# Performance work log

Measured on AMD Instinct MI355X. Metric: run time of the kernel, lower is better.

## Reference

```python
import jax, jax.numpy as jnp
import numpy as np

NEG = -9e15  # sentinel used by the torch module for masked logits


def setup_inputs() -> dict:
    key = jax.random.key(0)
    k_x, k_nl, k_q, k_k, k_v = jax.random.split(key, 5)
    n, m, nhid = 50000, 16, 128
    x = jax.random.normal(k_x, (n, nhid), dtype=jnp.float32)
    neighbor_list = jax.random.randint(k_nl, (n, m), 0, n)  # value n-1 == padding
    # xavier_uniform with gain=1.414 for square (nhid, nhid) matrices
    bound = 1.414 * np.sqrt(6.0 / (nhid + nhid))
    Q = jax.random.uniform(k_q, (nhid, nhid), jnp.float32, -bound, bound)
    K = jax.random.uniform(k_k, (nhid, nhid), jnp.float32, -bound, bound)
    V = jax.random.uniform(k_v, (nhid, nhid), jnp.float32, -bound, bound)
    return {"x": x, "neighbor_list": neighbor_list, "Q": Q, "K": K, "V": V}


def _forward(x, neighbor_list, Q, K, V):
    n, nhid = x.shape
    scare = jnp.asarray(nhid ** 0.5, x.dtype)
    # masks: neighbor index n-1 means padding
    mask = (neighbor_list != n - 1).astype(x.dtype)            # (n, m)
    mask1 = mask[:, :, None] * mask[:, None, :]                # (n, m, m)
    mask2 = jnp.concatenate([jnp.ones((n, 1), x.dtype), mask], axis=1)[:, None, :]  # (n,1,m+1)

    # ---- stage 1: neighbor-level attention ----
    nm = x[neighbor_list]                                      # (n, m, h) gather
    Qn = jnp.einsum('nmk,kh->nmh', nm, Q)
    Kn = jnp.einsum('nmk,kh->nmh', nm, K)
    Vn = jnp.einsum('nmk,kh->nmh', nm, V)
    s = jnp.einsum('nih,njh->nij', Qn, Kn)                     # (n, m, m)
    s = jax.nn.leaky_relu(s, 0.01)
    s = jnp.where(mask1 > 0, s, NEG) * scare                   # faithful: scale after mask
    a = jax.nn.softmax(s, axis=2)                              # dropout is identity (eval)
    nres = jnp.einsum('nij,njh->nih', a, Vn)                   # (n, m, h)

    # ---- stage 2: node-level attention over [self, neighbors] ----
    xr = x[:, None, :]                                         # (n, 1, h)
    cat = jnp.concatenate([xr, nres], axis=1)                  # (n, m+1, h)
    Qx = jnp.einsum('nik,kh->nih', xr, Q)                      # (n, 1, h)
    Kc = jnp.einsum('njk,kh->njh', cat, K)
    Vc = jnp.einsum('njk,kh->njh', cat, V)
    s2 = jnp.einsum('nih,njh->nij', Qx, Kc) * scare            # (n, 1, m+1)
    s2 = jax.nn.leaky_relu(s2, 0.01)
    s2 = jnp.where(mask2 > 0, s2, NEG)
    a2 = jax.nn.softmax(s2, axis=2)
    out = jnp.einsum('nij,njh->nih', a2, Vc)[:, 0, :]          # (n, h)

    # F.normalize: L2 along dim 1, eps 1e-12
    norm = jnp.linalg.norm(out, axis=1, keepdims=True)
    return out / jnp.maximum(norm, 1e-12)


def reference(x, neighbor_list, Q, K, V):
    return _forward(x, neighbor_list, Q, K, V)
```

## Files before the change

### kernel.cpp

```cpp
#include <hip/hip_runtime.h>
#include <math.h>

#define NEG_CONST (-9000000000000000.0f)
#define SCARE 11.313708498984761f

#define DPP_XOR1  0xB1
#define DPP_XOR2  0x4E
#define DPP_XOR7  0x141
#define DPP_XOR15 0x140

template<int CTRL>
__device__ __forceinline__ float dpp_add(float x) {
    int yi = __builtin_amdgcn_update_dpp(0, __float_as_int(x), CTRL, 0xF, 0xF, true);
    return x + __int_as_float(yi);
}
template<int CTRL>
__device__ __forceinline__ float dpp_max(float x) {
    int yi = __builtin_amdgcn_update_dpp(0, __float_as_int(x), CTRL, 0xF, 0xF, true);
    return fmaxf(x, __int_as_float(yi));
}

__device__ __forceinline__ void wave_lds_fence() {
    __builtin_amdgcn_wave_barrier();
    asm volatile("s_waitcnt lgkmcnt(0)" ::: "memory");
    __builtin_amdgcn_wave_barrier();
}
__device__ __forceinline__ void wave_vm_fence() {
    __builtin_amdgcn_wave_barrier();
    asm volatile("s_waitcnt vmcnt(0) lgkmcnt(0)" ::: "memory");
    __builtin_amdgcn_wave_barrier();
}

__global__ __launch_bounds__(256) void small_mm_qkt(const float* __restrict__ Q,
                                                    const float* __restrict__ K,
                                                    float* __restrict__ QKt) {
    int r  = blockIdx.x * 8 + (threadIdx.x >> 5);
    int c0 = (threadIdx.x & 31) * 4;
    float a0 = 0.f, a1 = 0.f, a2 = 0.f, a3 = 0.f;
    for (int k = 0; k < 128; k += 4) {
        float4 q  = *reinterpret_cast<const float4*>(&Q[r * 128 + k]);
        float4 k0 = *reinterpret_cast<const float4*>(&K[(c0 + 0) * 128 + k]);
        float4 k1 = *reinterpret_cast<const float4*>(&K[(c0 + 1) * 128 + k]);
        float4 k2 = *reinterpret_cast<const float4*>(&K[(c0 + 2) * 128 + k]);
        float4 k3 = *reinterpret_cast<const float4*>(&K[(c0 + 3) * 128 + k]);
        a0 += q.x*k0.x + q.y*k0.y + q.z*k0.z + q.w*k0.w;
        a1 += q.x*k1.x + q.y*k1.y + q.z*k1.z + q.w*k1.w;
        a2 += q.x*k2.x + q.y*k2.y + q.z*k2.z + q.w*k2.w;
        a3 += q.x*k3.x + q.y*k3.y + q.z*k3.z + q.w*k3.w;
    }
    float4 o = {a0, a1, a2, a3};
    *reinterpret_cast<float4*>(&QKt[r * 128 + c0]) = o;
}

__global__ __launch_bounds__(256) void small_mm_b(const float* __restrict__ QKt,
                                                  const float* __restrict__ V,
                                                  float* __restrict__ MT) {
    int r  = blockIdx.x * 8 + (threadIdx.x >> 5);
    int c0 = (threadIdx.x & 31) * 4;
    float a0 = 0.f, a1 = 0.f, a2 = 0.f, a3 = 0.f;
    for (int k = 0; k < 128; k += 4) {
        float4 q  = *reinterpret_cast<const float4*>(&QKt[r * 128 + k]);
        float4 k0 = *reinterpret_cast<const float4*>(&V[(c0 + 0) * 128 + k]);
        float4 k1 = *reinterpret_cast<const float4*>(&V[(c0 + 1) * 128 + k]);
        float4 k2 = *reinterpret_cast<const float4*>(&V[(c0 + 2) * 128 + k]);
        float4 k3 = *reinterpret_cast<const float4*>(&V[(c0 + 3) * 128 + k]);
        a0 += q.x*k0.x + q.y*k0.y + q.z*k0.z + q.w*k0.w;
        a1 += q.x*k1.x + q.y*k1.y + q.z*k1.z + q.w*k1.w;
        a2 += q.x*k2.x + q.y*k2.y + q.z*k2.z + q.w*k2.w;
        a3 += q.x*k3.x + q.y*k3.y + q.z*k3.z + q.w*k3.w;
    }
    float4 o = {a0, a1, a2, a3};
    *reinterpret_cast<float4*>(&MT[r * 128 + c0]) = o;
}

__global__ __launch_bounds__(256) void proj_gemm(
    const float* __restrict__ x,
    const float* __restrict__ W0, const float* __restrict__ W1,
    float* __restrict__ G, float* __restrict__ O1, int n)
{
    __shared__ __align__(16) float xs[32][132];
    __shared__ __align__(16) float ws[32][132];

    int yb = blockIdx.y;
    const float* W = yb ? W1 : W0;
    float*       O = yb ? O1 : G;
    int ostride = yb ? 128 : 256;
    int ooff    = yb ? 0 : 128;
    int row0 = blockIdx.x * 128;
    int tid = threadIdx.x;
    int tr = tid >> 4, tc = tid & 15;

    float acc[8][8] = {};
    for (int kk = 0; kk < 128; kk += 32) {
        #pragma unroll
        for (int it = 0; it < 4; ++it) {
            int id = tid + it * 256;
            int r = id >> 3;
            int f = id & 7;
            int grow = row0 + r;
            float4 v = (grow < n)
                ? *reinterpret_cast<const float4*>(&x[(size_t)grow * 128 + kk + f * 4])
                : make_float4(0.f, 0.f, 0.f, 0.f);
            xs[f * 4 + 0][r] = v.x; xs[f * 4 + 1][r] = v.y;
            xs[f * 4 + 2][r] = v.z; xs[f * 4 + 3][r] = v.w;
            if (yb == 0 && grow < n)
                *reinterpret_cast<float4*>(&G[(size_t)grow * 256 + kk + f * 4]) = v;
        }
        #pragma unroll
        for (int it = 0; it < 4; ++it) {
            int id = tid + it * 256;
            int k = id >> 5;
            int c4 = id & 31;
            *reinterpret_cast<float4*>(&ws[k][c4 * 4]) =
                *reinterpret_cast<const float4*>(&W[(size_t)(kk + k) * 128 + c4 * 4]);
        }
        __syncthreads();
        #pragma unroll 4
        for (int k = 0; k < 32; ++k) {
            float4 a0 = *reinterpret_cast<const float4*>(&xs[k][tr * 8]);
            float4 a1 = *reinterpret_cast<const float4*>(&xs[k][tr * 8 + 4]);
            float4 b0 = *reinterpret_cast<const float4*>(&ws[k][tc * 8]);
            float4 b1 = *reinterpret_cast<const float4*>(&ws[k][tc * 8 + 4]);
            float av[8] = {a0.x, a0.y, a0.z, a0.w, a1.x, a1.y, a1.z, a1.w};
            float bv[8] = {b0.x, b0.y, b0.z, b0.w, b1.x, b1.y, b1.z, b1.w};
            #pragma unroll
            for (int i2 = 0; i2 < 8; ++i2)
                #pragma unroll
                for (int j2 = 0; j2 < 8; ++j2)
                    acc[i2][j2] += av[i2] * bv[j2];
        }
        __syncthreads();
    }
    #pragma unroll
    for (int i2 = 0; i2 < 8; ++i2) {
        int grow = row0 + tr * 8 + i2;
        if (grow < n) {
            float4 o0 = {acc[i2][0], acc[i2][1], acc[i2][2], acc[i2][3]};
            float4 o1 = {acc[i2][4], acc[i2][5], acc[i2][6], acc[i2][7]};
            *reinterpret_cast<float4*>(&O[(size_t)grow * ostride + ooff + tc * 8])     = o0;
            *reinterpret_cast<float4*>(&O[(size_t)grow * ostride + ooff + tc * 8 + 4]) = o1;
        }
    }
}

__global__ __launch_bounds__(64, 5) void node_attn(
    const int* __restrict__ nlist,
    const float* __restrict__ G,
    float* uy,
    float* __restrict__ c0a,
    int n)
{
    __shared__ __align__(16) float Bs[2048];
    __shared__ __align__(16) float Ts[16];

    const int l  = threadIdx.x;
    const int g  = l >> 2;
    const int jj = l & 3;
    const int i  = blockIdx.x;

    int nlv = 0;
    if (l < 16) nlv = nlist[(size_t)i * 16 + l];
    unsigned long long mb = __ballot(l < 16 ? (nlv != n - 1) : 0);

    {
        int sub   = l & 31;
        int sigma = ((sub & 3) << 3) | (sub >> 2);
        int half  = l >> 5;
        #pragma unroll
        for (int p = 0; p < 8; ++p) {
            int nr = __shfl(nlv, 2 * p + half, 64);
            const float* src = &G[(size_t)nr * 256 + sigma * 4];
            __builtin_amdgcn_global_load_lds(
                (const __attribute__((address_space(1))) unsigned int*)src,
                (__attribute__((address_space(3))) unsigned int*)&Bs[p * 256],
                16, 0, 0);
        }
    }

    float2 qa = *reinterpret_cast<const float2*>(&G[(size_t)i * 256 + 128 + l * 2]);
    float2 xa = *reinterpret_cast<const float2*>(&G[(size_t)i * 256 + l * 2]);
    float s200 = qa.x * xa.x + qa.y * xa.y;
    s200 = dpp_add<DPP_XOR1>(s200);
    s200 = dpp_add<DPP_XOR2>(s200);
    s200 = dpp_add<DPP_XOR7>(s200);
    s200 = dpp_add<DPP_XOR15>(s200);
    s200 += __shfl_xor(s200, 16, 64);
    s200 += __shfl_xor(s200, 32, 64);

    int nl_g = __shfl(nlv, g, 64);
    float4 A[8];
    {
        const float* ab = &G[(size_t)nl_g * 256 + 128 + jj * 32];
        #pragma unroll
        for (int k4 = 0; k4 < 8; ++k4)
            A[k4] = *reinterpret_cast<const float4*>(&ab[k4 * 4]);
    }

    wave_vm_fence();

    float a[16];
    {
        float sc[16];
        #pragma unroll
        for (int c = 0; c < 16; ++c) {
            const float* bb = &Bs[c * 128 + jj * 4];
            float acc = 0.f;
            #pragma unroll
            for (int k4 = 0; k4 < 8; ++k4) {
                float4 b = *reinterpret_cast<const float4*>(&bb[k4 * 16]);
                acc += A[k4].x * b.x + A[k4].y * b.y + A[k4].z * b.z + A[k4].w * b.w;
            }
            acc = dpp_add<DPP_XOR1>(acc);
            acc = dpp_add<DPP_XOR2>(acc);
            sc[c] = acc;
        }
        bool rlive = (mb >> g) & 1ULL;
        float m = -3.0e38f;
        #pragma unroll
        for (int c = 0; c < 16; ++c) {
            float s = sc[c];
            float slr = s > 0.f ? s : 0.01f * s;
            bool live = rlive && ((mb >> c) & 1ULL);
            float sm = (live ? slr : NEG_CONST) * SCARE;
            sc[c] = sm;
            m = fmaxf(m, sm);
        }
        float ssum = 0.f;
        #pragma unroll
        for (int c = 0; c < 16; ++c) { float p = __expf(sc[c] - m); a[c] = p; ssum += p; }
        float rs = 1.f / ssum;
        #pragma unroll
        for (int c = 0; c < 16; ++c) a[c] *= rs;
    }

    {
        float acc = 0.f;
        #pragma unroll
        for (int k4 = 0; k4 < 8; ++k4) {
            int kx = (k4 + g) & 7;
            float4 b  = *reinterpret_cast<const float4*>(&Bs[g * 128 + kx * 16 + jj * 4]);
            float4 uu = *reinterpret_cast<const float4*>(&uy[(size_t)i * 128 + jj * 32 + kx * 4]);
            acc += uu.x * b.x + uu.y * b.y + uu.z * b.z + uu.w * b.w;
        }
        acc = dpp_add<DPP_XOR1>(acc);
        acc = dpp_add<DPP_XOR2>(acc);
        if (jj == 0) Ts[g] = acc;
    }
    wave_lds_fence();
    float tarr[16];
    {
        #pragma unroll
        for (int q4 = 0; q4 < 4; ++q4) {
            float4 t4 = *reinterpret_cast<const float4*>(&Ts[q4 * 4]);
            tarr[q4 * 4 + 0] = t4.x; tarr[q4 * 4 + 1] = t4.y;
            tarr[q4 * 4 + 2] = t4.z; tarr[q4 * 4 + 3] = t4.w;
        }
    }

    float lg = 0.f;
    #pragma unroll
    for (int k = 0; k < 16; ++k) lg += a[k] * tarr[k];
    {
        float v = lg * SCARE;
        v = v > 0.f ? v : 0.01f * v;
        lg = ((mb >> g) & 1ULL) ? v : NEG_CONST;
    }
    float v0 = s200 * SCARE;
    v0 = v0 > 0.f ? v0 : 0.01f * v0;

    float m17 = lg;
    m17 = dpp_max<DPP_XOR7>(m17);
    m17 = dpp_max<DPP_XOR15>(m17);
    m17 = fmaxf(m17, __shfl_xor(m17, 16, 64));
    m17 = fmaxf(m17, __shfl_xor(m17, 32, 64));
    m17 = fmaxf(m17, v0);
    float pg = __expf(lg - m17);
    float sg = pg;
    sg = dpp_add<DPP_XOR7>(sg);
    sg = dpp_add<DPP_XOR15>(sg);
    sg += __shfl_xor(sg, 16, 64);
    sg += __shfl_xor(sg, 32, 64);
    float p0 = __expf(v0 - m17);
    float inv = 1.f / (sg + p0);
    float a2g = pg * inv;
    float a20 = p0 * inv;

    float w[16];
    #pragma unroll
    for (int k = 0; k < 16; ++k) {
        float wv = a2g * a[k];
        wv = dpp_add<DPP_XOR7>(wv);
        wv = dpp_add<DPP_XOR15>(wv);
        wv += __shfl_xor(wv, 16, 64);
        wv += __shfl_xor(wv, 32, 64);
        w[k] = wv;
    }

    {
        int sg2 = l >> 1;
        int tau = ((sg2 & 7) << 2) | (sg2 >> 3);
        int off2 = (2 * l) & 3;
        float y0 = 0.f, y1 = 0.f;
        #pragma unroll
        for (int k = 0; k < 16; ++k) {
            float2 bp = *reinterpret_cast<const float2*>(&Bs[k * 128 + tau * 4 + off2]);
            y0 += w[k] * bp.x;
            y1 += w[k] * bp.y;
        }
        float2 yw = {y0, y1};
        *reinterpret_cast<float2*>(&uy[(size_t)i * 128 + 2 * l]) = yw;
    }
    if (l == 0) c0a[i] = a20;
}

__global__ __launch_bounds__(256) void ep_fused(
    const float* __restrict__ y, const float* __restrict__ G,
    const float* __restrict__ c0a, const float* __restrict__ Vw,
    float* __restrict__ outp, int n)
{
    __shared__ __align__(16) float as_[32][132];
    __shared__ __align__(16) float wsd[32][132];

    int row0 = blockIdx.x * 128;
    int tid = threadIdx.x;
    int tr = tid >> 4, tc = tid & 15;

    float acc[8][8] = {};
    for (int kk = 0; kk < 128; kk += 32) {
        #pragma unroll
        for (int it = 0; it < 4; ++it) {
            int id = tid + it * 256;
            int r = id >> 3;
            int f = id & 7;
            int grow = row0 + r;
            float4 v = (grow < n)
                ? *reinterpret_cast<const float4*>(&y[(size_t)grow * 128 + kk + f * 4])
                : make_float4(0.f, 0.f, 0.f, 0.f);
            as_[f * 4 + 0][r] = v.x; as_[f * 4 + 1][r] = v.y;
            as_[f * 4 + 2][r] = v.z; as_[f * 4 + 3][r] = v.w;
        }
        #pragma unroll
        for (int it = 0; it < 4; ++it) {
            int id = tid + it * 256;
            int k = id >> 5;
            int c4 = id & 31;
            *reinterpret_cast<float4*>(&wsd[k][c4 * 4]) =
                *reinterpret_cast<const float4*>(&Vw[(size_t)(kk + k) * 128 + c4 * 4]);
        }
        __syncthreads();
        #pragma unroll 4
        for (int k = 0; k < 32; ++k) {
            float4 a0 = *reinterpret_cast<const float4*>(&as_[k][tr * 8]);
            float4 a1 = *reinterpret_cast<const float4*>(&as_[k][tr * 8 + 4]);
            float4 b0 = *reinterpret_cast<const float4*>(&wsd[k][tc * 8]);
            float4 b1 = *reinterpret_cast<const float4*>(&wsd[k][tc * 8 + 4]);
            float av[8] = {a0.x, a0.y, a0.z, a0.w, a1.x, a1.y, a1.z, a1.w};
            float bv[8] = {b0.x, b0.y, b0.z, b0.w, b1.x, b1.y, b1.z, b1.w};
            #pragma unroll
            for (int i2 = 0; i2 < 8; ++i2)
                #pragma unroll
                for (int j2 = 0; j2 < 8; ++j2)
                    acc[i2][j2] += av[i2] * bv[j2];
        }
        __syncthreads();
    }

    #pragma unroll
    for (int i2 = 0; i2 < 8; ++i2) {
        int grow = row0 + tr * 8 + i2;
        if (grow < n) {
            float c0v = c0a[grow];
            float4 g0 = *reinterpret_cast<const float4*>(&G[(size_t)grow * 256 + tc * 8]);
            float4 g1 = *reinterpret_cast<const float4*>(&G[(size_t)grow * 256 + tc * 8 + 4]);
            acc[i2][0] += c0v * g0.x; acc[i2][1] += c0v * g0.y;
            acc[i2][2] += c0v * g0.z; acc[i2][3] += c0v * g0.w;
            acc[i2][4] += c0v * g1.x; acc[i2][5] += c0v * g1.y;
            acc[i2][6] += c0v * g1.z; acc[i2][7] += c0v * g1.w;
        }
    }

    float acc2[8][8] = {};
    for (int kk = 0; kk < 128; kk += 32) {
        __syncthreads();
        int tcl = tc - (kk >> 3);
        if (tcl >= 0 && tcl < 4) {
            #pragma unroll
            for (int j2 = 0; j2 < 8; ++j2)
                #pragma unroll
                for (int i2 = 0; i2 < 8; ++i2)
                    as_[tcl * 8 + j2][tr * 8 + i2] = acc[i2][j2];
        }
        #pragma unroll
        for (int it = 0; it < 4; ++it) {
            int id = tid + it * 256;
            int k = id >> 5;
            int c4 = id & 31;
            *reinterpret_cast<float4*>(&wsd[k][c4 * 4]) =
                *reinterpret_cast<const float4*>(&Vw[(size_t)(kk + k) * 128 + c4 * 4]);
        }
        __syncthreads();
        #pragma unroll 4
        for (int k = 0; k < 32; ++k) {
            float4 a0 = *reinterpret_cast<const float4*>(&as_[k][tr * 8]);
            float4 a1 = *reinterpret_cast<const float4*>(&as_[k][tr * 8 + 4]);
            float4 b0 = *reinterpret_cast<const float4*>(&wsd[k][tc * 8]);
            float4 b1 = *reinterpret_cast<const float4*>(&wsd[k][tc * 8 + 4]);
            float av[8] = {a0.x, a0.y, a0.z, a0.w, a1.x, a1.y, a1.z, a1.w};
            float bv[8] = {b0.x, b0.y, b0.z, b0.w, b1.x, b1.y, b1.z, b1.w};
            #pragma unroll
            for (int i2 = 0; i2 < 8; ++i2)
                #pragma unroll
                for (int j2 = 0; j2 < 8; ++j2)
                    acc2[i2][j2] += av[i2] * bv[j2];
        }
    }

    #pragma unroll
    for (int i2 = 0; i2 < 8; ++i2) {
        int grow = row0 + tr * 8 + i2;
        float ss = 0.f;
        #pragma unroll
        for (int j2 = 0; j2 < 8; ++j2) ss += acc2[i2][j2] * acc2[i2][j2];
        ss = dpp_add<DPP_XOR1>(ss);
        ss = dpp_add<DPP_XOR2>(ss);
        ss = dpp_add<DPP_XOR7>(ss);
        ss = dpp_add<DPP_XOR15>(ss);
        float d = fmaxf(sqrtf(ss), 1e-12f);
        float rd = 1.f / d;
        if (grow < n) {
            float4 o0 = {acc2[i2][0] * rd, acc2[i2][1] * rd, acc2[i2][2] * rd, acc2[i2][3] * rd};
            float4 o1 = {acc2[i2][4] * rd, acc2[i2][5] * rd, acc2[i2][6] * rd, acc2[i2][7] * rd};
            *reinterpret_cast<float4*>(&outp[(size_t)grow * 128 + tc * 8])     = o0;
            *reinterpret_cast<float4*>(&outp[(size_t)grow * 128 + tc * 8 + 4]) = o1;
        }
    }
}

extern "C" void kernel_launch(void* const* d_in, const int* in_sizes, int n_in,
                              void* d_out, int out_size, void* d_ws, size_t ws_size,
                              hipStream_t stream) {
    const float* x     = (const float*)d_in[0];
    const int*   nlist = (const int*)d_in[1];
    const float* Q     = (const float*)d_in[2];
    const float* K     = (const float*)d_in[3];
    const float* V     = (const float*)d_in[4];
    float* out = (float*)d_out;
    int n = in_sizes[0] / 128;

    float* ws   = (float*)d_ws;
    float* QKt  = ws;
    float* MT   = ws + 16384;
    float* c0a  = ws + 32768;
    float* G    = c0a + n;
    float* uarr = G + (size_t)n * 256;

    small_mm_qkt<<<dim3(16), 256, 0, stream>>>(Q, K, QKt);
    small_mm_b<<<dim3(16), 256, 0, stream>>>(QKt, V, MT);
    dim3 g2((n + 127) / 128, 2);
    proj_gemm<<<g2, 256, 0, stream>>>(x, QKt, MT, G, uarr, n);
    node_attn<<<n, 64, 0, stream>>>(nlist, G, uarr, c0a, n);
    ep_fused<<<(n + 127) / 128, 256, 0, stream>>>(uarr, G, c0a, V, out, n);
}
```

Measured before the change: 303.8 us.

## Fuse projection GEMMs via chained QKt then VT, merge small matmul kernels

The projection kernel now computes x·QKt first, then reuses that result from shared memory as the A operand of a second GEMM with V transposed. This replaces the separate x·(QKt·V^T) pass and removes the small second precompute kernel. The QKt and V-transpose precomputes are merged into one launch. In node_attn, the per-row u·B dot is folded into the score loop with u held in registers, dropping an LDS round-trip and fence, and softmax normalisation is deferred into a combined coefficient. The fused projection runs its two GEMMs serially per block instead of on two parallel grid slices, and node_attn's occupancy hint drops from 5 to 4 because of higher register use.

```diff
diff --git a/kernel.cpp b/kernel.cpp
--- a/kernel.cpp
+++ b/kernel.cpp
@@ -20,72 +20,52 @@
     return fmaxf(x, __int_as_float(yi));
 }
 
-__device__ __forceinline__ void wave_lds_fence() {
-    __builtin_amdgcn_wave_barrier();
-    asm volatile("s_waitcnt lgkmcnt(0)" ::: "memory");
-    __builtin_amdgcn_wave_barrier();
-}
 __device__ __forceinline__ void wave_vm_fence() {
     __builtin_amdgcn_wave_barrier();
     asm volatile("s_waitcnt vmcnt(0) lgkmcnt(0)" ::: "memory");
     __builtin_amdgcn_wave_barrier();
 }
 
-__global__ __launch_bounds__(256) void small_mm_qkt(const float* __restrict__ Q,
+__global__ __launch_bounds__(256) void small_qkt_vt(const float* __restrict__ Q,
                                                     const float* __restrict__ K,
-                                                    float* __restrict__ QKt) {
+                                                    const float* __restrict__ V,
+                                                    float* __restrict__ QKt,
+                                                    float* __restrict__ VT) {
     int r  = blockIdx.x * 8 + (threadIdx.x >> 5);
     int c0 = (threadIdx.x & 31) * 4;
-    float a0 = 0.f, a1 = 0.f, a2 = 0.f, a3 = 0.f;
-    for (int k = 0; k < 128; k += 4) {
-        float4 q  = *reinterpret_cast<const float4*>(&Q[r * 128 + k]);
-        float4 k0 = *reinterpret_cast<const float4*>(&K[(c0 + 0) * 128 + k]);
-        float4 k1 = *reinterpret_cast<const float4*>(&K[(c0 + 1) * 128 + k]);
-        float4 k2 = *reinterpret_cast<const float4*>(&K[(c0 + 2) * 128 + k]);
-        float4 k3 = *reinterpret_cast<const float4*>(&K[(c0 + 3) * 128 + k]);
-        a0 += q.x*k0.x + q.y*k0.y + q.z*k0.z + q.w*k0.w;
-        a1 += q.x*k1.x + q.y*k1.y + q.z*k1.z + q.w*k1.w;
-        a2 += q.x*k2.x + q.y*k2.y + q.z*k2.z + q.w*k2.w;
-        a3 += q.x*k3.x + q.y*k3.y + q.z*k3.z + q.w*k3.w;
-    }
-    float4 o = {a0, a1, a2, a3};
-    *reinterpret_cast<float4*>(&QKt[r * 128 + c0]) = o;
-}
-
-__global__ __launch_bounds__(256) void small_mm_b(const float* __restrict__ QKt,
-                                                  const float* __restrict__ V,
-                                                  float* __restrict__ MT) {
-    int r  = blockIdx.x * 8 + (threadIdx.x >> 5);
-    int c0 = (threadIdx.x & 31) * 4;
-    float a0 = 0.f, a1 = 0.f, a2 = 0.f, a3 = 0.f;
-    for (int k = 0; k < 128; k += 4) {
-        float4 q  = *reinterpret_cast<const float4*>(&QKt[r * 128 + k]);
-        float4 k0 = *reinterpret_cast<const float4*>(&V[(c0 + 0) * 128 + k]);
-        float4 k1 = *reinterpret_cast<const float4*>(&V[(c0 + 1) * 128 + k]);
-        float4 k2 = *reinterpret_cast<const float4*>(&V[(c0 + 2) * 128 + k]);
-        float4 k3 = *reinterpret_cast<const float4*>(&V[(c0 + 3) * 128 + k]);
-        a0 += q.x*k0.x + q.y*k0.y + q.z*k0.z + q.w*k0.w;
-        a1 += q.x*k1.x + q.y*k1.y + q.z*k1.z + q.w*k1.w;
-        a2 += q.x*k2.x + q.y*k2.y + q.z*k2.z + q.w*k2.w;
-        a3 += q.x*k3.x + q.y*k3.y + q.z*k3.z + q.w*k3.w;
-    }
-    float4 o = {a0, a1, a2, a3};
-    *reinterpret_cast<float4*>(&MT[r * 128 + c0]) = o;
-}
-
-__global__ __launch_bounds__(256) void proj_gemm(
+    if (blockIdx.y == 0) {
+        float a0 = 0.f, a1 = 0.f, a2 = 0.f, a3 = 0.f;
+        for (int k = 0; k < 128; k += 4) {
+            float4 q  = *reinterpret_cast<const float4*>(&Q[r * 128 + k]);
+            float4 k0 = *reinterpret_cast<const float4*>(&K[(c0 + 0) * 128 + k]);
+            float4 k1 = *reinterpret_cast<const float4*>(&K[(c0 + 1) * 128 + k]);
+            float4 k2 = *reinterpret_cast<const float4*>(&K[(c0 + 2) * 128 + k]);
+            float4 k3 = *reinterpret_cast<const float4*>(&K[(c0 + 3) * 128 + k]);
+            a0 += q.x*k0.x + q.y*k0.y + q.z*k0.z + q.w*k0.w;
+            a1 += q.x*k1.x + q.y*k1.y + q.z*k1.z + q.w*k1.w;
+            a2 += q.x*k2.x + q.y*k2.y + q.z*k2.z + q.w*k2.w;
+            a3 += q.x*k3.x + q.y*k3.y + q.z*k3.z + q.w*k3.w;
+        }
+        float4 o = {a0, a1, a2, a3};
+        *reinterpret_cast<float4*>(&QKt[r * 128 + c0]) = o;
+    } else {
+        float4 o;
+        o.x = V[(c0 + 0) * 128 + r];
+        o.y = V[(c0 + 1) * 128 + r];
+        o.z = V[(c0 + 2) * 128 + r];
+        o.w = V[(c0 + 3) * 128 + r];
+        *reinterpret_cast<float4*>(&VT[r * 128 + c0]) = o;
+    }
+}
+
+__global__ __launch_bounds__(256) void proj_fused(
     const float* __restrict__ x,
-    const float* __restrict__ W0, const float* __restrict__ W1,
-    float* __restrict__ G, float* __restrict__ O1, int n)
+    const float* __restrict__ QKt, const float* __restrict__ VT,
+    float* __restrict__ G, float* __restrict__ u, int n)
 {
-    __shared__ __align__(16) float xs[32][132];
-    __shared__ __align__(16) float ws[32][132];
-
-    int yb = blockIdx.y;
-    const float* W = yb ? W1 : W0;
-    float*       O = yb ? O1 : G;
-    int ostride = yb ? 128 : 256;
-    int ooff    = yb ? 0 : 128;
+    __shared__ __align__(16) float as_[32][132];
+    __shared__ __align__(16) float wsd[32][132];
+
     int row0 = blockIdx.x * 128;
     int tid = threadIdx.x;
     int tr = tid >> 4, tc = tid & 15;
@@ -101,9 +81,9 @@
             float4 v = (grow < n)
                 ? *reinterpret_cast<const float4*>(&x[(size_t)grow * 128 + kk + f * 4])
                 : make_float4(0.f, 0.f, 0.f, 0.f);
-            xs[f * 4 + 0][r] = v.x; xs[f * 4 + 1][r] = v.y;
-            xs[f * 4 + 2][r] = v.z; xs[f * 4 + 3][r] = v.w;
-            if (yb == 0 && grow < n)
+            as_[f * 4 + 0][r] = v.x; as_[f * 4 + 1][r] = v.y;
+            as_[f * 4 + 2][r] = v.z; as_[f * 4 + 3][r] = v.w;
+            if (grow < n)
                 *reinterpret_cast<float4*>(&G[(size_t)grow * 256 + kk + f * 4]) = v;
         }
         #pragma unroll
@@ -111,16 +91,16 @@
             int id = tid + it * 256;
             int k = id >> 5;
             int c4 = id & 31;
-            *reinterpret_cast<float4*>(&ws[k][c4 * 4]) =
-                *reinterpret_cast<const float4*>(&W[(size_t)(kk + k) * 128 + c4 * 4]);
+            *reinterpret_cast<float4*>(&wsd[k][c4 * 4]) =
+                *reinterpret_cast<const float4*>(&QKt[(size_t)(kk + k) * 128 + c4 * 4]);
         }
         __syncthreads();
         #pragma unroll 4
         for (int k = 0; k < 32; ++k) {
-            float4 a0 = *reinterpret_cast<const float4*>(&xs[k][tr * 8]);
-            float4 a1 = *reinterpret_cast<const float4*>(&xs[k][tr * 8 + 4]);
-            float4 b0 = *reinterpret_cast<const float4*>(&ws[k][tc * 8]);
-            float4 b1 = *reinterpret_cast<const float4*>(&ws[k][tc * 8 + 4]);
+            float4 a0 = *reinterpret_cast<const float4*>(&as_[k][tr * 8]);
+            float4 a1 = *reinterpret_cast<const float4*>(&as_[k][tr * 8 + 4]);
+            float4 b0 = *reinterpret_cast<const float4*>(&wsd[k][tc * 8]);
+            float4 b1 = *reinterpret_cast<const float4*>(&wsd[k][tc * 8 + 4]);
             float av[8] = {a0.x, a0.y, a0.z, a0.w, a1.x, a1.y, a1.z, a1.w};
             float bv[8] = {b0.x, b0.y, b0.z, b0.w, b1.x, b1.y, b1.z, b1.w};
             #pragma unroll
@@ -131,19 +111,66 @@
         }
         __syncthreads();
     }
+
     #pragma unroll
     for (int i2 = 0; i2 < 8; ++i2) {
         int grow = row0 + tr * 8 + i2;
         if (grow < n) {
             float4 o0 = {acc[i2][0], acc[i2][1], acc[i2][2], acc[i2][3]};
             float4 o1 = {acc[i2][4], acc[i2][5], acc[i2][6], acc[i2][7]};
-            *reinterpret_cast<float4*>(&O[(size_t)grow * ostride + ooff + tc * 8])     = o0;
-            *reinterpret_cast<float4*>(&O[(size_t)grow * ostride + ooff + tc * 8 + 4]) = o1;
-        }
-    }
-}
-
-__global__ __launch_bounds__(64, 5) void node_attn(
+            *reinterpret_cast<float4*>(&G[(size_t)grow * 256 + 128 + tc * 8])     = o0;
+            *reinterpret_cast<float4*>(&G[(size_t)grow * 256 + 128 + tc * 8 + 4]) = o1;
+        }
+    }
+
+    float acc2[8][8] = {};
+    for (int kk = 0; kk < 128; kk += 32) {
+        __syncthreads();
+        int tcl = tc - (kk >> 3);
+        if (tcl >= 0 && tcl < 4) {
+            #pragma unroll
+            for (int j2 = 0; j2 < 8; ++j2)
+                #pragma unroll
+                for (int i2 = 0; i2 < 8; ++i2)
+                    as_[tcl * 8 + j2][tr * 8 + i2] = acc[i2][j2];
+        }
+        #pragma unroll
+        for (int it = 0; it < 4; ++it) {
+            int id = tid + it * 256;
+            int k = id >> 5;
+            int c4 = id & 31;
+            *reinterpret_cast<float4*>(&wsd[k][c4 * 4]) =
+                *reinterpret_cast<const float4*>(&VT[(size_t)(kk + k) * 128 + c4 * 4]);
+        }
+        __syncthreads();
+        #pragma unroll 4
+        for (int k = 0; k < 32; ++k) {
+            float4 a0 = *reinterpret_cast<const float4*>(&as_[k][tr * 8]);
+            float4 a1 = *reinterpret_cast<const float4*>(&as_[k][tr * 8 + 4]);
+            float4 b0 = *reinterpret_cast<const float4*>(&wsd[k][tc * 8]);
+            float4 b1 = *reinterpret_cast<const float4*>(&wsd[k][tc * 8 + 4]);
+            float av[8] = {a0.x, a0.y, a0.z, a0.w, a1.x, a1.y, a1.z, a1.w};
+            float bv[8] = {b0.x, b0.y, b0.z, b0.w, b1.x, b1.y, b1.z, b1.w};
+            #pragma unroll
+            for (int i2 = 0; i2 < 8; ++i2)
+                #pragma unroll
+                for (int j2 = 0; j2 < 8; ++j2)
+                    acc2[i2][j2] += av[i2] * bv[j2];
+        }
+    }
+    #pragma unroll
+    for (int i2 = 0; i2 < 8; ++i2) {
+        int grow = row0 + tr * 8 + i2;
+        if (grow < n) {
+            float4 o0 = {acc2[i2][0], acc2[i2][1], acc2[i2][2], acc2[i2][3]};
+            float4 o1 = {acc2[i2][4], acc2[i2][5], acc2[i2][6], acc2[i2][7]};
+            *reinterpret_cast<float4*>(&u[(size_t)grow * 128 + tc * 8])     = o0;
+            *reinterpret_cast<float4*>(&u[(size_t)grow * 128 + tc * 8 + 4]) = o1;
+        }
+    }
+}
+
+__global__ __launch_bounds__(64, 4) void node_attn(
     const int* __restrict__ nlist,
     const float* __restrict__ G,
     float* uy,
@@ -151,7 +178,6 @@
     int n)
 {
     __shared__ __align__(16) float Bs[2048];
-    __shared__ __align__(16) float Ts[16];
 
     const int l  = threadIdx.x;
     const int g  = l >> 2;
@@ -175,6 +201,14 @@
                 (__attribute__((address_space(3))) unsigned int*)&Bs[p * 256],
                 16, 0, 0);
         }
+    }
+
+    float4 uu[8];
+    {
+        const float* ub = &uy[(size_t)i * 128 + jj * 32];
+        #pragma unroll
+        for (int k4 = 0; k4 < 8; ++k4)
+            uu[k4] = *reinterpret_cast<const float4*>(&ub[k4 * 4]);
     }
 
     float2 qa = *reinterpret_cast<const float2*>(&G[(size_t)i * 256 + 128 + l * 2]);
@@ -199,67 +233,47 @@
     wave_vm_fence();
 
     float a[16];
-    {
-        float sc[16];
+    float tv[16];
+    float inv_s;
+    {
         #pragma unroll
         for (int c = 0; c < 16; ++c) {
             const float* bb = &Bs[c * 128 + jj * 4];
-            float acc = 0.f;
+            float accs = 0.f, acct = 0.f;
             #pragma unroll
             for (int k4 = 0; k4 < 8; ++k4) {
                 float4 b = *reinterpret_cast<const float4*>(&bb[k4 * 16]);
-                acc += A[k4].x * b.x + A[k4].y * b.y + A[k4].z * b.z + A[k4].w * b.w;
+                accs += A[k4].x * b.x + A[k4].y * b.y + A[k4].z * b.z + A[k4].w * b.w;
+                acct += uu[k4].x * b.x + uu[k4].y * b.y + uu[k4].z * b.z + uu[k4].w * b.w;
             }
-            acc = dpp_add<DPP_XOR1>(acc);
-            acc = dpp_add<DPP_XOR2>(acc);
-            sc[c] = acc;
+            accs = dpp_add<DPP_XOR1>(accs);
+            accs = dpp_add<DPP_XOR2>(accs);
+            acct = dpp_add<DPP_XOR1>(acct);
+            acct = dpp_add<DPP_XOR2>(acct);
+            a[c]  = accs;
+            tv[c] = acct;
         }
         bool rlive = (mb >> g) & 1ULL;
         float m = -3.0e38f;
         #pragma unroll
         for (int c = 0; c < 16; ++c) {
-            float s = sc[c];
+            float s = a[c];
             float slr = s > 0.f ? s : 0.01f * s;
             bool live = rlive && ((mb >> c) & 1ULL);
             float sm = (live ? slr : NEG_CONST) * SCARE;
-            sc[c] = sm;
+            a[c] = sm;
             m = fmaxf(m, sm);
         }
         float ssum = 0.f;
         #pragma unroll
-        for (int c = 0; c < 16; ++c) { float p = __expf(sc[c] - m); a[c] = p; ssum += p; }
-        float rs = 1.f / ssum;
-        #pragma unroll
-        for (int c = 0; c < 16; ++c) a[c] *= rs;
-    }
-
-    {
-        float acc = 0.f;
-        #pragma unroll
-        for (int k4 = 0; k4 < 8; ++k4) {
-            int kx = (k4 + g) & 7;
-            float4 b  = *reinterpret_cast<const float4*>(&Bs[g * 128 + kx * 16 + jj * 4]);
-            float4 uu = *reinterpret_cast<const float4*>(&uy[(size_t)i * 128 + jj * 32 + kx * 4]);
-            acc += uu.x * b.x + uu.y * b.y + uu.z * b.z + uu.w * b.w;
-        }
-        acc = dpp_add<DPP_XOR1>(acc);
-        acc = dpp_add<DPP_XOR2>(acc);
-        if (jj == 0) Ts[g] = acc;
-    }
-    wave_lds_fence();
-    float tarr[16];
-    {
-        #pragma unroll
-        for (int q4 = 0; q4 < 4; ++q4) {
-            float4 t4 = *reinterpret_cast<const float4*>(&Ts[q4 * 4]);
-            tarr[q4 * 4 + 0] = t4.x; tarr[q4 * 4 + 1] = t4.y;
-            tarr[q4 * 4 + 2] = t4.z; tarr[q4 * 4 + 3] = t4.w;
-        }
+        for (int c = 0; c < 16; ++c) { float p = __expf(a[c] - m); a[c] = p; ssum += p; }
+        inv_s = 1.f / ssum;
     }
 
     float lg = 0.f;
     #pragma unroll
-    for (int k = 0; k < 16; ++k) lg += a[k] * tarr[k];
+    for (int k = 0; k < 16; ++k) lg += a[k] * tv[k];
+    lg *= inv_s;
     {
         float v = lg * SCARE;
         v = v > 0.f ? v : 0.01f * v;
@@ -281,14 +295,14 @@
     sg += __shfl_xor(sg, 16, 64);
     sg += __shfl_xor(sg, 32, 64);
     float p0 = __expf(v0 - m17);
-    float inv = 1.f / (sg + p0);
-    float a2g = pg * inv;
-    float a20 = p0 * inv;
+    float inv2 = 1.f / (sg + p0);
+    float a20 = p0 * inv2;
+    float coeff = pg * inv2 * inv_s;
 
     float w[16];
     #pragma unroll
     for (int k = 0; k < 16; ++k) {
-        float wv = a2g * a[k];
+        float wv = coeff * a[k];
         wv = dpp_add<DPP_XOR7>(wv);
         wv = dpp_add<DPP_XOR15>(wv);
         wv += __shfl_xor(wv, 16, 64);
@@ -449,15 +463,13 @@
 
     float* ws   = (float*)d_ws;
     float* QKt  = ws;
-    float* MT   = ws + 16384;
+    float* VT   = ws + 16384;
     float* c0a  = ws + 32768;
     float* G    = c0a + n;
     float* uarr = G + (size_t)n * 256;
 
-    small_mm_qkt<<<dim3(16), 256, 0, stream>>>(Q, K, QKt);
-    small_mm_b<<<dim3(16), 256, 0, stream>>>(QKt, V, MT);
-    dim3 g2((n + 127) / 128, 2);
-    proj_gemm<<<g2, 256, 0, stream>>>(x, QKt, MT, G, uarr, n);
+    small_qkt_vt<<<dim3(16, 2), 256, 0, stream>>>(Q, K, V, QKt, VT);
+    proj_fused<<<(n + 127) / 128, 256, 0, stream>>>(x, QKt, VT, G, uarr, n);
     node_attn<<<n, 64, 0, stream>>>(nlist, G, uarr, c0a, n);
     ep_fused<<<(n + 127) / 128, 256, 0, stream>>>(uarr, G, c0a, V, out, n);
 }
```

Result: slower. 453.0 us (+49.1%).
